# Kernel tuning notes

Hardware: AMD Instinct MI355X
Metric: run time of the kernel (lower is better)

The kernel has to match this reference:

```python
import jax, jax.numpy as jnp
import numpy as np

B, T, V, E, U = 64, 4995, 4096, 100, 64


def gru_layer(x, W, R, b, return_sequences):
    """Keras GRU (reset_after=True). x: [B,T,D]. Returns [B,T,U] or [B,U]."""
    u = R.shape[0]
    # Precompute all input projections in one big matmul: [B,T,3u]
    xp = jnp.einsum('btd,dk->btk', x, W) + b[0]
    h0 = jnp.zeros((x.shape[0], u), dtype=x.dtype)

    def step(h, xt):
        hp = h @ R + b[1]                                   # [B,3u]
        z = jax.nn.sigmoid(xt[:, :u] + hp[:, :u])
        r = jax.nn.sigmoid(xt[:, u:2 * u] + hp[:, u:2 * u])
        hh = jnp.tanh(xt[:, 2 * u:] + r * hp[:, 2 * u:])
        h_new = z * h + (1.0 - z) * hh
        return h_new, (h_new if return_sequences else None)

    hT, ys = jax.lax.scan(step, h0, jnp.swapaxes(xp, 0, 1))  # scan over time
    if return_sequences:
        return jnp.swapaxes(ys, 0, 1)                        # [B,T,U]
    return hT                                                # [B,U]


def setup_inputs() -> dict:
    key = jax.random.key(0)
    ks = jax.random.split(key, 8)
    s = 0.05
    return {
        'tokens': jax.random.randint(ks[0], (B, T), 0, V, dtype=jnp.int32),
        'emb': jax.random.normal(ks[1], (V, E), jnp.float32) * s,
        'W1': jax.random.normal(ks[2], (E, 3 * U), jnp.float32) * s,
        'U1': jax.random.normal(ks[3], (U, 3 * U), jnp.float32) * s,
        'b1': jnp.zeros((2, 3 * U), jnp.float32),
        'W2': jax.random.normal(ks[4], (U, 3 * U), jnp.float32) * s,
        'U2': jax.random.normal(ks[5], (U, 3 * U), jnp.float32) * s,
        'b2': jnp.zeros((2, 3 * U), jnp.float32),
        'Wout': jax.random.normal(ks[6], (U, 1), jnp.float32) * s,
        'bout': jnp.zeros((1,), jnp.float32),
    }


def reference(tokens, emb, W1, U1, b1, W2, U2, b2, Wout, bout):
    x = emb[tokens]                                   # [B,T,E] embedding lookup
    x = gru_layer(x, W1, U1, b1, return_sequences=True)   # [B,T,U]
    h = gru_layer(x, W2, U2, b2, return_sequences=False)  # [B,U] (last state)
    logits = h @ Wout + bout                          # [B,1]
    return jax.nn.sigmoid(logits)
```

## Files before the change

kernel.cpp:

```cpp
#include <hip/hip_runtime.h>

#define BB 64
#define TT 4995
#define VV 4096
#define EE 100
#define UU 64
#define U3 192
#define BPB 4
#define NBLK (BB / BPB)

using bf16x8 = __attribute__((ext_vector_type(8))) short;
using f32x4  = __attribute__((ext_vector_type(4))) float;

#define MFMA16 __builtin_amdgcn_mfma_f32_16x16x32_bf16

#define LDS_BARRIER()                                   \
    do {                                                \
        __builtin_amdgcn_sched_barrier(0);              \
        asm volatile("s_waitcnt lgkmcnt(0)" ::: "memory"); \
        __builtin_amdgcn_s_barrier();                   \
        __builtin_amdgcn_sched_barrier(0);              \
    } while (0)

__device__ float g_embW[VV * U3];

__device__ __forceinline__ float fast_sigmoid(float x) {
    return __builtin_amdgcn_rcpf(1.0f + __expf(-x));
}
__device__ __forceinline__ float fast_tanh(float x) {
    return __builtin_amdgcn_rcpf(1.0f + __expf(-2.0f * x)) * 2.0f - 1.0f;
}
__device__ __forceinline__ unsigned short f2bf(float f) {
    unsigned u = __float_as_uint(f);
    return (unsigned short)((u + 0x7FFFu + ((u >> 16) & 1u)) >> 16);
}
__device__ __forceinline__ float bf2f(unsigned short h) {
    return __uint_as_float(((unsigned)h) << 16);
}

__global__ void gru_embw_kernel(const float* __restrict__ emb,
                                const float* __restrict__ W1,
                                const float* __restrict__ b1) {
    __shared__ float row[EE];
    const int v = blockIdx.x;
    const int k = threadIdx.x;
    if (k < EE) row[k] = emb[v * EE + k];
    __syncthreads();
    float acc = b1[k];
    #pragma unroll 4
    for (int j = 0; j < EE; ++j)
        acc = fmaf(row[j], W1[j * U3 + k], acc);
    g_embW[v * U3 + k] = acc;
}

__global__ __launch_bounds__(512, 1)
void gru_scan_kernel(const int* __restrict__ tokens,
                     const float* __restrict__ U1,
                     const float* __restrict__ b1,
                     const float* __restrict__ W2,
                     const float* __restrict__ U2,
                     const float* __restrict__ b2,
                     const float* __restrict__ Wout,
                     const float* __restrict__ bout,
                     float* __restrict__ out) {
    const int blk  = blockIdx.x;
    const int tid  = threadIdx.x;
    const int wave = tid >> 6;
    const int lane = tid & 63;
    const int lg   = lane >> 4;
    const int lc   = lane & 15;
    const bool isL2 = (wave >= 4);
    const int ut   = wave & 3;

    __shared__ __align__(16) char hls[8192];
    for (int i = tid; i < 2048; i += 512) ((int*)hls)[i] = 0;

    bf16x8 fb[12];
    const int cz = ut * 16 + lc;
    const int cr = 64 + ut * 16 + lc;
    const int ch = 128 + ut * 16 + lc;
    {
        const float* M0 = isL2 ? W2 : U1;
        #pragma unroll
        for (int g = 0; g < 3; ++g) {
            const int col = g * 64 + ut * 16 + lc;
            #pragma unroll
            for (int kk = 0; kk < 2; ++kk) {
                bf16x8 v;
                #pragma unroll
                for (int e = 0; e < 8; ++e)
                    v[e] = (short)f2bf(M0[(8 * lg + 32 * kk + e) * U3 + col]);
                fb[g * 2 + kk] = v;
            }
        }
        if (isL2) {
            #pragma unroll
            for (int g = 0; g < 3; ++g) {
                const int col = g * 64 + ut * 16 + lc;
                #pragma unroll
                for (int kk = 0; kk < 2; ++kk) {
                    bf16x8 v;
                    #pragma unroll
                    for (int e = 0; e < 8; ++e)
                        v[e] = (short)f2bf(U2[(8 * lg + 32 * kk + e) * U3 + col]);
                    fb[6 + g * 2 + kk] = v;
                }
            }
        } else {
            #pragma unroll
            for (int q = 6; q < 12; ++q) fb[q] = fb[q - 6];
        }
    }

    float bias_z, bias_r, bias_h, bias_h2 = 0.0f;
    if (!isL2) {
        bias_z = b1[U3 + cz]; bias_r = b1[U3 + cr]; bias_h = b1[U3 + ch];
    } else {
        bias_z  = b2[cz] + b2[U3 + cz];
        bias_r  = b2[cr] + b2[U3 + cr];
        bias_h  = b2[ch];
        bias_h2 = b2[U3 + ch];
    }
    const f32x4 bz4 = {bias_z, bias_z, bias_z, bias_z};
    const f32x4 br4 = {bias_r, bias_r, bias_r, bias_r};
    const f32x4 bh4 = {bias_h, bias_h, bias_h, bias_h};
    const f32x4 bp4 = {bias_h2, bias_h2, bias_h2, bias_h2};
    const f32x4 zq  = {0.0f, 0.0f, 0.0f, 0.0f};

    float xp[4][3];
    int   tok[4];
    const int rowbase = (blk * BPB + lg) * TT;
    if (!isL2) {
        const int t0 = tokens[rowbase];
        const int t1 = tokens[rowbase + 1];
        tok[2] = tokens[rowbase + 2];
        tok[3] = tokens[rowbase + 3];
        tok[0] = 0; tok[1] = 0;
        xp[0][0] = g_embW[t0 * U3 + cz];
        xp[0][1] = g_embW[t0 * U3 + cr];
        xp[0][2] = g_embW[t0 * U3 + ch];
        xp[1][0] = g_embW[t1 * U3 + cz];
        xp[1][1] = g_embW[t1 * U3 + cr];
        xp[1][2] = g_embW[t1 * U3 + ch];
        #pragma unroll
        for (int q = 2; q < 4; ++q)
            xp[q][0] = xp[q][1] = xp[q][2] = 0.0f;
    }

    float h1o = 0.0f;
    float h2o = 0.0f;

    __syncthreads();

    const int swzA = (lc & 7) << 4;
    const int myrow = 4 * lg;
    const int wswz  = ((myrow & 7) << 4);
    const int wbyte = myrow * 128 + (((ut * 16 + lc) * 2) ^ wswz);

    #pragma unroll 1
    for (int sq = 0; sq < TT + 1; sq += 4) {
        #pragma unroll
        for (int ph = 0; ph < 4; ++ph) {
            const int s = sq + ph;
            char* rdb = hls + (ph & 1) * 4096;
            char* wrb = hls + ((ph & 1) ^ 1) * 4096;

            if (!isL2) {
                const int tn = tok[(ph + 2) & 3];
                xp[(ph + 2) & 3][0] = g_embW[tn * U3 + cz];
                xp[(ph + 2) & 3][1] = g_embW[tn * U3 + cr];
                xp[(ph + 2) & 3][2] = g_embW[tn * U3 + ch];
                const int s4 = (s + 4 < TT) ? (s + 4) : (TT - 1);
                tok[ph & 3] = tokens[rowbase + s4];

                bf16x8 a1_0 = *(const bf16x8*)(rdb + lc * 128 + ((16 * lg) ^ swzA));
                bf16x8 a1_1 = *(const bf16x8*)(rdb + lc * 128 + ((16 * lg + 64) ^ swzA));

                if (s < TT) {
                    f32x4 az = MFMA16(a1_0, fb[0], bz4, 0, 0, 0);
                    az       = MFMA16(a1_1, fb[1], az,  0, 0, 0);
                    f32x4 ar = MFMA16(a1_0, fb[2], br4, 0, 0, 0);
                    ar       = MFMA16(a1_1, fb[3], ar,  0, 0, 0);
                    f32x4 ah = MFMA16(a1_0, fb[4], bh4, 0, 0, 0);
                    ah       = MFMA16(a1_1, fb[5], ah,  0, 0, 0);
                    const float z  = fast_sigmoid(xp[ph][0] + az[0]);
                    const float rg = fast_sigmoid(xp[ph][1] + ar[0]);
                    const float hh = fast_tanh(xp[ph][2] + rg * ah[0]);
                    h1o = fmaf(z, h1o - hh, hh);
                    *(unsigned short*)(wrb + wbyte) = f2bf(h1o);
                }
            } else {
                bf16x8 a1_0 = *(const bf16x8*)(rdb + lc * 128 + ((16 * lg) ^ swzA));
                bf16x8 a1_1 = *(const bf16x8*)(rdb + lc * 128 + ((16 * lg + 64) ^ swzA));
                bf16x8 a2_0 = *(const bf16x8*)(rdb + 2048 + lc * 128 + ((16 * lg) ^ swzA));
                bf16x8 a2_1 = *(const bf16x8*)(rdb + 2048 + lc * 128 + ((16 * lg + 64) ^ swzA));

                if (s > 0) {
                    f32x4 az1 = MFMA16(a1_0, fb[0],  bz4, 0, 0, 0);
                    az1       = MFMA16(a1_1, fb[1],  az1, 0, 0, 0);
                    f32x4 az2 = MFMA16(a2_0, fb[6],  zq,  0, 0, 0);
                    az2       = MFMA16(a2_1, fb[7],  az2, 0, 0, 0);
                    f32x4 ar1 = MFMA16(a1_0, fb[2],  br4, 0, 0, 0);
                    ar1       = MFMA16(a1_1, fb[3],  ar1, 0, 0, 0);
                    f32x4 ar2 = MFMA16(a2_0, fb[8],  zq,  0, 0, 0);
                    ar2       = MFMA16(a2_1, fb[9],  ar2, 0, 0, 0);
                    f32x4 ax  = MFMA16(a1_0, fb[4],  bh4, 0, 0, 0);
                    ax        = MFMA16(a1_1, fb[5],  ax,  0, 0, 0);
                    f32x4 ap  = MFMA16(a2_0, fb[10], bp4, 0, 0, 0);
                    ap        = MFMA16(a2_1, fb[11], ap,  0, 0, 0);
                    const float z  = fast_sigmoid(az1[0] + az2[0]);
                    const float rg = fast_sigmoid(ar1[0] + ar2[0]);
                    const float hh = fast_tanh(ax[0] + rg * ap[0]);
                    h2o = fmaf(z, h2o - hh, hh);
                    *(unsigned short*)(wrb + 2048 + wbyte) = f2bf(h2o);
                }
            }
            LDS_BARRIER();
        }
    }

    if (wave == 0 && lane < BPB) {
        const int row = 4 * lane;
        float acc = bout[0];
        #pragma unroll 8
        for (int u = 0; u < UU; ++u) {
            const unsigned short hv = *(const unsigned short*)(hls + 2048 +
                row * 128 + ((u * 2) ^ ((row & 7) << 4)));
            acc = fmaf(bf2f(hv), Wout[u], acc);
        }
        out[blk * BPB + lane] = fast_sigmoid(acc);
    }
}

extern "C" void kernel_launch(void* const* d_in, const int* in_sizes, int n_in,
                              void* d_out, int out_size, void* d_ws, size_t ws_size,
                              hipStream_t stream) {
    const int*   tokens = (const int*)  d_in[0];
    const float* emb    = (const float*)d_in[1];
    const float* W1     = (const float*)d_in[2];
    const float* U1w    = (const float*)d_in[3];
    const float* b1     = (const float*)d_in[4];
    const float* W2     = (const float*)d_in[5];
    const float* U2w    = (const float*)d_in[6];
    const float* b2     = (const float*)d_in[7];
    const float* Wout   = (const float*)d_in[8];
    const float* bout   = (const float*)d_in[9];
    float* out = (float*)d_out;

    gru_embw_kernel<<<VV, 192, 0, stream>>>(emb, W1, b1);
    gru_scan_kernel<<<NBLK, 512, 0, stream>>>(tokens, U1w, b1, W2, U2w,
                                              b2, Wout, bout, out);
}
```

Before: 1.645 ms.

## Merge layer-1 and layer-2 GRU waves so each wave computes both layers

Each block drops from 512 to 256 threads. Every wave now runs both the layer-1 and the layer-2 recurrence step for its 16 output units, where before layer 1 and layer 2 ran on separate wave groups. Fewer waves meet at each per-step barrier, which should lower synchronisation cost on this latency-bound serial scan. In exchange each wave issues the MFMAs and transcendentals for both layers back to back and holds more weight fragments in registers, which lengthens the per-step critical path.

```diff
diff --git a/kernel.cpp b/kernel.cpp
--- a/kernel.cpp
+++ b/kernel.cpp
@@ -53,7 +53,7 @@
     g_embW[v * U3 + k] = acc;
 }
 
-__global__ __launch_bounds__(512, 1)
+__global__ __launch_bounds__(256, 1)
 void gru_scan_kernel(const int* __restrict__ tokens,
                      const float* __restrict__ U1,
                      const float* __restrict__ b1,
@@ -65,35 +65,22 @@
                      float* __restrict__ out) {
     const int blk  = blockIdx.x;
     const int tid  = threadIdx.x;
-    const int wave = tid >> 6;
     const int lane = tid & 63;
     const int lg   = lane >> 4;
     const int lc   = lane & 15;
-    const bool isL2 = (wave >= 4);
-    const int ut   = wave & 3;
+    const int ut   = tid >> 6;
 
     __shared__ __align__(16) char hls[8192];
-    for (int i = tid; i < 2048; i += 512) ((int*)hls)[i] = 0;
-
-    bf16x8 fb[12];
+    for (int i = tid; i < 2048; i += 256) ((int*)hls)[i] = 0;
+
+    bf16x8 fb[18];
     const int cz = ut * 16 + lc;
     const int cr = 64 + ut * 16 + lc;
     const int ch = 128 + ut * 16 + lc;
     {
-        const float* M0 = isL2 ? W2 : U1;
+        const float* Ms[3] = {U1, W2, U2};
         #pragma unroll
-        for (int g = 0; g < 3; ++g) {
-            const int col = g * 64 + ut * 16 + lc;
-            #pragma unroll
-            for (int kk = 0; kk < 2; ++kk) {
-                bf16x8 v;
-                #pragma unroll
-                for (int e = 0; e < 8; ++e)
-                    v[e] = (short)f2bf(M0[(8 * lg + 32 * kk + e) * U3 + col]);
-                fb[g * 2 + kk] = v;
-            }
-        }
-        if (isL2) {
+        for (int m = 0; m < 3; ++m) {
             #pragma unroll
             for (int g = 0; g < 3; ++g) {
                 const int col = g * 64 + ut * 16 + lc;
@@ -102,35 +89,31 @@
                     bf16x8 v;
                     #pragma unroll
                     for (int e = 0; e < 8; ++e)
-                        v[e] = (short)f2bf(U2[(8 * lg + 32 * kk + e) * U3 + col]);
-                    fb[6 + g * 2 + kk] = v;
+                        v[e] = (short)f2bf(Ms[m][(8 * lg + 32 * kk + e) * U3 + col]);
+                    fb[m * 6 + g * 2 + kk] = v;
                 }
             }
-        } else {
-            #pragma unroll
-            for (int q = 6; q < 12; ++q) fb[q] = fb[q - 6];
         }
     }
 
-    float bias_z, bias_r, bias_h, bias_h2 = 0.0f;
-    if (!isL2) {
-        bias_z = b1[U3 + cz]; bias_r = b1[U3 + cr]; bias_h = b1[U3 + ch];
-    } else {
-        bias_z  = b2[cz] + b2[U3 + cz];
-        bias_r  = b2[cr] + b2[U3 + cr];
-        bias_h  = b2[ch];
-        bias_h2 = b2[U3 + ch];
-    }
-    const f32x4 bz4 = {bias_z, bias_z, bias_z, bias_z};
-    const f32x4 br4 = {bias_r, bias_r, bias_r, bias_r};
-    const f32x4 bh4 = {bias_h, bias_h, bias_h, bias_h};
-    const f32x4 bp4 = {bias_h2, bias_h2, bias_h2, bias_h2};
-    const f32x4 zq  = {0.0f, 0.0f, 0.0f, 0.0f};
+    const float bz1 = b1[U3 + cz], br1 = b1[U3 + cr], bh1 = b1[U3 + ch];
+    const float bz2 = b2[cz] + b2[U3 + cz];
+    const float br2 = b2[cr] + b2[U3 + cr];
+    const float bx2 = b2[ch];
+    const float bp2 = b2[U3 + ch];
+    const f32x4 bz14 = {bz1, bz1, bz1, bz1};
+    const f32x4 br14 = {br1, br1, br1, br1};
+    const f32x4 bh14 = {bh1, bh1, bh1, bh1};
+    const f32x4 bz24 = {bz2, bz2, bz2, bz2};
+    const f32x4 br24 = {br2, br2, br2, br2};
+    const f32x4 bx24 = {bx2, bx2, bx2, bx2};
+    const f32x4 bp24 = {bp2, bp2, bp2, bp2};
+    const f32x4 zq   = {0.0f, 0.0f, 0.0f, 0.0f};
 
     float xp[4][3];
     int   tok[4];
     const int rowbase = (blk * BPB + lg) * TT;
-    if (!isL2) {
+    {
         const int t0 = tokens[rowbase];
         const int t1 = tokens[rowbase + 1];
         tok[2] = tokens[rowbase + 2];
@@ -165,61 +148,56 @@
             char* rdb = hls + (ph & 1) * 4096;
             char* wrb = hls + ((ph & 1) ^ 1) * 4096;
 
-            if (!isL2) {
-                const int tn = tok[(ph + 2) & 3];
-                xp[(ph + 2) & 3][0] = g_embW[tn * U3 + cz];
-                xp[(ph + 2) & 3][1] = g_embW[tn * U3 + cr];
-                xp[(ph + 2) & 3][2] = g_embW[tn * U3 + ch];
-                const int s4 = (s + 4 < TT) ? (s + 4) : (TT - 1);
-                tok[ph & 3] = tokens[rowbase + s4];
-
-                bf16x8 a1_0 = *(const bf16x8*)(rdb + lc * 128 + ((16 * lg) ^ swzA));
-                bf16x8 a1_1 = *(const bf16x8*)(rdb + lc * 128 + ((16 * lg + 64) ^ swzA));
-
-                if (s < TT) {
-                    f32x4 az = MFMA16(a1_0, fb[0], bz4, 0, 0, 0);
-                    az       = MFMA16(a1_1, fb[1], az,  0, 0, 0);
-                    f32x4 ar = MFMA16(a1_0, fb[2], br4, 0, 0, 0);
-                    ar       = MFMA16(a1_1, fb[3], ar,  0, 0, 0);
-                    f32x4 ah = MFMA16(a1_0, fb[4], bh4, 0, 0, 0);
-                    ah       = MFMA16(a1_1, fb[5], ah,  0, 0, 0);
-                    const float z  = fast_sigmoid(xp[ph][0] + az[0]);
-                    const float rg = fast_sigmoid(xp[ph][1] + ar[0]);
-                    const float hh = fast_tanh(xp[ph][2] + rg * ah[0]);
-                    h1o = fmaf(z, h1o - hh, hh);
-                    *(unsigned short*)(wrb + wbyte) = f2bf(h1o);
-                }
-            } else {
-                bf16x8 a1_0 = *(const bf16x8*)(rdb + lc * 128 + ((16 * lg) ^ swzA));
-                bf16x8 a1_1 = *(const bf16x8*)(rdb + lc * 128 + ((16 * lg + 64) ^ swzA));
-                bf16x8 a2_0 = *(const bf16x8*)(rdb + 2048 + lc * 128 + ((16 * lg) ^ swzA));
-                bf16x8 a2_1 = *(const bf16x8*)(rdb + 2048 + lc * 128 + ((16 * lg + 64) ^ swzA));
-
-                if (s > 0) {
-                    f32x4 az1 = MFMA16(a1_0, fb[0],  bz4, 0, 0, 0);
-                    az1       = MFMA16(a1_1, fb[1],  az1, 0, 0, 0);
-                    f32x4 az2 = MFMA16(a2_0, fb[6],  zq,  0, 0, 0);
-                    az2       = MFMA16(a2_1, fb[7],  az2, 0, 0, 0);
-                    f32x4 ar1 = MFMA16(a1_0, fb[2],  br4, 0, 0, 0);
-                    ar1       = MFMA16(a1_1, fb[3],  ar1, 0, 0, 0);
-                    f32x4 ar2 = MFMA16(a2_0, fb[8],  zq,  0, 0, 0);
-                    ar2       = MFMA16(a2_1, fb[9],  ar2, 0, 0, 0);
-                    f32x4 ax  = MFMA16(a1_0, fb[4],  bh4, 0, 0, 0);
-                    ax        = MFMA16(a1_1, fb[5],  ax,  0, 0, 0);
-                    f32x4 ap  = MFMA16(a2_0, fb[10], bp4, 0, 0, 0);
-                    ap        = MFMA16(a2_1, fb[11], ap,  0, 0, 0);
-                    const float z  = fast_sigmoid(az1[0] + az2[0]);
-                    const float rg = fast_sigmoid(ar1[0] + ar2[0]);
-                    const float hh = fast_tanh(ax[0] + rg * ap[0]);
-                    h2o = fmaf(z, h2o - hh, hh);
-                    *(unsigned short*)(wrb + 2048 + wbyte) = f2bf(h2o);
-                }
+            const int tn = tok[(ph + 2) & 3];
+            xp[(ph + 2) & 3][0] = g_embW[tn * U3 + cz];
+            xp[(ph + 2) & 3][1] = g_embW[tn * U3 + cr];
+            xp[(ph + 2) & 3][2] = g_embW[tn * U3 + ch];
+            const int s4 = (s + 4 < TT) ? (s + 4) : (TT - 1);
+            tok[ph & 3] = tokens[rowbase + s4];
+
+            bf16x8 a1_0 = *(const bf16x8*)(rdb + lc * 128 + ((16 * lg) ^ swzA));
+            bf16x8 a1_1 = *(const bf16x8*)(rdb + lc * 128 + ((16 * lg + 64) ^ swzA));
+            bf16x8 a2_0 = *(const bf16x8*)(rdb + 2048 + lc * 128 + ((16 * lg) ^ swzA));
+            bf16x8 a2_1 = *(const bf16x8*)(rdb + 2048 + lc * 128 + ((16 * lg + 64) ^ swzA));
+
+            if (s < TT) {
+                f32x4 az = MFMA16(a1_0, fb[0], bz14, 0, 0, 0);
+                az       = MFMA16(a1_1, fb[1], az,   0, 0, 0);
+                f32x4 ar = MFMA16(a1_0, fb[2], br14, 0, 0, 0);
+                ar       = MFMA16(a1_1, fb[3], ar,   0, 0, 0);
+                f32x4 ah = MFMA16(a1_0, fb[4], bh14, 0, 0, 0);
+                ah       = MFMA16(a1_1, fb[5], ah,   0, 0, 0);
+                const float z  = fast_sigmoid(xp[ph][0] + az[0]);
+                const float rg = fast_sigmoid(xp[ph][1] + ar[0]);
+                const float hh = fast_tanh(xp[ph][2] + rg * ah[0]);
+                h1o = fmaf(z, h1o - hh, hh);
+                *(unsigned short*)(wrb + wbyte) = f2bf(h1o);
+            }
+
+            if (s > 0) {
+                f32x4 az1 = MFMA16(a1_0, fb[6],  bz24, 0, 0, 0);
+                az1       = MFMA16(a1_1, fb[7],  az1,  0, 0, 0);
+                f32x4 az2 = MFMA16(a2_0, fb[12], zq,   0, 0, 0);
+                az2       = MFMA16(a2_1, fb[13], az2,  0, 0, 0);
+                f32x4 ar1 = MFMA16(a1_0, fb[8],  br24, 0, 0, 0);
+                ar1       = MFMA16(a1_1, fb[9],  ar1,  0, 0, 0);
+                f32x4 ar2 = MFMA16(a2_0, fb[14], zq,   0, 0, 0);
+                ar2       = MFMA16(a2_1, fb[15], ar2,  0, 0, 0);
+                f32x4 ax  = MFMA16(a1_0, fb[10], bx24, 0, 0, 0);
+                ax        = MFMA16(a1_1, fb[11], ax,   0, 0, 0);
+                f32x4 ap  = MFMA16(a2_0, fb[16], bp24, 0, 0, 0);
+                ap        = MFMA16(a2_1, fb[17], ap,   0, 0, 0);
+                const float z  = fast_sigmoid(az1[0] + az2[0]);
+                const float rg = fast_sigmoid(ar1[0] + ar2[0]);
+                const float hh = fast_tanh(ax[0] + rg * ap[0]);
+                h2o = fmaf(z, h2o - hh, hh);
+                *(unsigned short*)(wrb + 2048 + wbyte) = f2bf(h2o);
             }
             LDS_BARRIER();
         }
     }
 
-    if (wave == 0 && lane < BPB) {
+    if (ut == 0 && lane < BPB) {
         const int row = 4 * lane;
         float acc = bout[0];
         #pragma unroll 8
@@ -248,6 +226,6 @@
     float* out = (float*)d_out;
 
     gru_embw_kernel<<<VV, 192, 0, stream>>>(emb, W1, b1);
-    gru_scan_kernel<<<NBLK, 512, 0, stream>>>(tokens, U1w, b1, W2, U2w,
+    gru_scan_kernel<<<NBLK, 256, 0, stream>>>(tokens, U1w, b1, W2, U2w,
                                               b2, Wout, bout, out);
 }
```

After: 2.019 ms. +22.7%, slower.
